# Optimization experiments

Hardware: AMD Instinct MI355X
Metric: run time of the kernel (lower is better)

The kernel has to match this reference:

```python
import jax, jax.numpy as jnp
import numpy as np

B, IN, H = 4096, 2048, 2048


def setup_inputs() -> dict:
    key = jax.random.key(0)
    ks = jax.random.split(key, 20)
    s_in = 1.0 / np.sqrt(IN)
    s_h = 1.0 / np.sqrt(H)
    inp = {
        "x": jax.random.normal(ks[0], (B, IN), jnp.float32),
        "h": jax.random.normal(ks[1], (B, H), jnp.float32),
        "c": jax.random.normal(ks[2], (B, H), jnp.float32),
    }
    names_in = [("Wii", "bii"), ("Wif", "bif"), ("Wig", "big"), ("Wio", "bio")]
    names_h = [("Whi", "bhi"), ("Whf", "bhf"), ("Whg", "bhg"), ("Who", "bho")]
    k = 3
    for wn, bn in names_in:
        inp[wn] = jax.random.normal(ks[k], (H, IN), jnp.float32) * s_in
        inp[bn] = jax.random.normal(ks[k + 1], (H,), jnp.float32) * s_in
        k += 2
    for wn, bn in names_h:
        inp[wn] = jax.random.normal(ks[k], (H, H), jnp.float32) * s_h
        inp[bn] = jax.random.normal(ks[k + 1], (H,), jnp.float32) * s_h
        k += 2
    return inp


def reference(x, h, c, Wii, bii, Whi, bhi, Wif, bif, Whf, bhf,
              Wig, big, Whg, bhg, Wio, bio, Who, bho):
    # Fuse the 4 input-projections and 4 hidden-projections into two GEMMs
    # (same math as 8 separate nn.Linear calls).
    Wx = jnp.concatenate([Wii, Wif, Wig, Wio], axis=0)   # [4H, IN]
    Wh = jnp.concatenate([Whi, Whf, Whg, Who], axis=0)   # [4H, H]
    bx = jnp.concatenate([bii, bif, big, bio])            # [4H]
    bh = jnp.concatenate([bhi, bhf, bhg, bho])            # [4H]
    gates = x @ Wx.T + h @ Wh.T + bx + bh                 # [B, 4H]
    ii, ff, gg, oo = jnp.split(gates, 4, axis=-1)
    i = jax.nn.sigmoid(ii)
    f = jax.nn.sigmoid(ff)
    g = jnp.tanh(gg)
    o = jax.nn.sigmoid(oo)
    c_new = f * c + i * g
    h_new = o * jnp.tanh(c_new)
    return jnp.stack([h_new, c_new])  # [2, B, H]
```

## Files before the change

### kernel.cpp

```cpp
#include <hip/hip_runtime.h>
#include <stdint.h>

typedef __attribute__((ext_vector_type(4))) float f32x4;
typedef __attribute__((ext_vector_type(8))) short bf16x8;

#define MFMA_BF16 __builtin_amdgcn_mfma_f32_16x16x32_bf16

__device__ __forceinline__ unsigned short f2bf(float f) {
  union { float f; uint32_t u; } a; a.f = f;
  uint32_t u = a.u;
  uint32_t r = (u + 0x7FFFu + ((u >> 16) & 1u)) >> 16;
  return (unsigned short)r;
}

__global__ void pack_a_kernel(const float4* __restrict__ x, const float4* __restrict__ hh,
                              ushort4* __restrict__ A) {
  const int total = 4096 * 1024;
  for (int q = blockIdx.x * blockDim.x + threadIdx.x; q < total; q += gridDim.x * blockDim.x) {
    int row = q >> 10, cq = q & 1023;
    float4 v = (cq < 512) ? x[row * 512 + cq] : hh[row * 512 + (cq - 512)];
    ushort4 o; o.x = f2bf(v.x); o.y = f2bf(v.y); o.z = f2bf(v.z); o.w = f2bf(v.w);
    A[q] = o;
  }
}

__global__ void pack_w_kernel(const float* __restrict__ Wii, const float* __restrict__ Wif,
                              const float* __restrict__ Wig, const float* __restrict__ Wio,
                              const float* __restrict__ Whi, const float* __restrict__ Whf,
                              const float* __restrict__ Whg, const float* __restrict__ Who,
                              ushort4* __restrict__ Wp) {
  const int total = 8192 * 1024;
  for (int q = blockIdx.x * blockDim.x + threadIdx.x; q < total; q += gridDim.x * blockDim.x) {
    int p = q >> 10, kq = q & 1023;
    int r = p & 255;
    int g = ((r >> 7) << 1) | ((r >> 4) & 1);
    int H = ((p >> 8) << 6) | (((r >> 5) & 3) << 4) | (r & 15);
    const float* src;
    if (kq < 512) src = (g == 0) ? Wii : (g == 1) ? Wif : (g == 2) ? Wig : Wio;
    else          src = (g == 0) ? Whi : (g == 1) ? Whf : (g == 2) ? Whg : Who;
    const float4 v = *(const float4*)&src[(size_t)H * 2048 + ((kq & 511) << 2)];
    ushort4 o; o.x = f2bf(v.x); o.y = f2bf(v.y); o.z = f2bf(v.z); o.w = f2bf(v.w);
    Wp[q] = o;
  }
}

#define STG(srcbase, jj, koff, dstE)                                                        \
  __builtin_amdgcn_global_load_lds(                                                        \
      (const __attribute__((address_space(1))) void*)((srcbase) + (size_t)(jj)*262144 + (koff)), \
      (__attribute__((address_space(3))) void*)(&smem[(dstE) + (jj)*4096]), 16, 0, 0)

__global__ __launch_bounds__(512, 2)
void lstm_gemm_kernel(const ushort* __restrict__ A, const ushort* __restrict__ Wp,
                      const float* __restrict__ c,
                      const float* __restrict__ bii, const float* __restrict__ bif_,
                      const float* __restrict__ big_, const float* __restrict__ bio_,
                      const float* __restrict__ bhi, const float* __restrict__ bhf,
                      const float* __restrict__ bhg, const float* __restrict__ bho,
                      float* __restrict__ out) {
  __shared__ ushort smem[65536];
  const int tid = threadIdx.x;
  const int lane = tid & 63, w = tid >> 6;
  const int wm = w >> 2, wn = w & 3;

  const int bid = blockIdx.x;
  const int xcd = bid & 7, q = bid >> 3;
  const int bn = (xcd << 2) | (q >> 4);
  const int bm = q & 15;

  const int laneRow = lane & 15, lane16 = lane >> 4;
  const int lr7 = laneRow & 7;
  const int colE0 = (lane16 ^ lr7) << 3;
  const int colE1 = ((4 + lane16) ^ lr7) << 3;

  const int srow = w * 8 + (lane >> 3);
  const int chunkOff = ((lane & 7) ^ (lane >> 3)) << 3;
  const ushort* aSrc = A + (size_t)(bm * 256 + srow) * 4096 + chunkOff;
  const ushort* bSrc = Wp + (size_t)(bn * 256 + srow) * 4096 + chunkOff;
  const int aDstW = w * 512;
  const int bDstW = 16384 + w * 512;

  const int aBase = (wm * 64 + laneRow) * 64;
  const int bBase = 16384 + (wn * 32 + laneRow) * 64;

  f32x4 acc[8][4];
#pragma unroll
  for (int i = 0; i < 8; i++)
#pragma unroll
    for (int j = 0; j < 4; j++) acc[i][j] = (f32x4){0.f, 0.f, 0.f, 0.f};

  STG(aSrc, 0, 0, aDstW); STG(aSrc, 1, 0, aDstW);
  STG(aSrc, 2, 0, aDstW); STG(aSrc, 3, 0, aDstW);
  STG(bSrc, 0, 0, bDstW); STG(bSrc, 1, 0, bDstW);
  STG(bSrc, 2, 0, bDstW); STG(bSrc, 3, 0, bDstW);
  asm volatile("s_waitcnt vmcnt(0)" ::: "memory");
  __builtin_amdgcn_s_barrier();
  __builtin_amdgcn_sched_barrier(0);

#pragma unroll 1
  for (int T = 0; T < 64; ++T) {
    const int bufE = (T & 1) << 15;
    const int obufE = bufE ^ 32768;
    const int kS = (T + 1) << 6;

    if (T < 63) {
      STG(aSrc, 0, kS, obufE + aDstW); STG(aSrc, 1, kS, obufE + aDstW);
      STG(aSrc, 2, kS, obufE + aDstW); STG(aSrc, 3, kS, obufE + aDstW);
      STG(bSrc, 0, kS, obufE + bDstW); STG(bSrc, 1, kS, obufE + bDstW);
      STG(bSrc, 2, kS, obufE + bDstW); STG(bSrc, 3, kS, obufE + bDstW);
    }

    bf16x8 af[4][2], b01[2][2], b23[2][2];
#pragma unroll
    for (int m = 0; m < 4; ++m) {
      af[m][0] = *(const bf16x8*)&smem[bufE + aBase + m * 1024 + colE0];
      af[m][1] = *(const bf16x8*)&smem[bufE + aBase + m * 1024 + colE1];
    }
#pragma unroll
    for (int n = 0; n < 2; ++n) {
      b01[n][0] = *(const bf16x8*)&smem[bufE + bBase + n * 1024 + colE0];
      b01[n][1] = *(const bf16x8*)&smem[bufE + bBase + n * 1024 + colE1];
    }
    __builtin_amdgcn_s_setprio(1);
#pragma unroll
    for (int m = 0; m < 4; ++m)
#pragma unroll
      for (int n = 0; n < 2; ++n) {
        acc[m][n] = MFMA_BF16(af[m][0], b01[n][0], acc[m][n], 0, 0, 0);
        acc[m][n] = MFMA_BF16(af[m][1], b01[n][1], acc[m][n], 0, 0, 0);
      }
    __builtin_amdgcn_s_setprio(0);

#pragma unroll
    for (int n = 0; n < 2; ++n) {
      b23[n][0] = *(const bf16x8*)&smem[bufE + bBase + 8192 + n * 1024 + colE0];
      b23[n][1] = *(const bf16x8*)&smem[bufE + bBase + 8192 + n * 1024 + colE1];
    }
    __builtin_amdgcn_s_setprio(1);
#pragma unroll
    for (int m = 0; m < 4; ++m)
#pragma unroll
      for (int n = 0; n < 2; ++n) {
        acc[m][2 + n] = MFMA_BF16(af[m][0], b23[n][0], acc[m][2 + n], 0, 0, 0);
        acc[m][2 + n] = MFMA_BF16(af[m][1], b23[n][1], acc[m][2 + n], 0, 0, 0);
      }
    __builtin_amdgcn_s_setprio(0);

#pragma unroll
    for (int m = 0; m < 4; ++m) {
      af[m][0] = *(const bf16x8*)&smem[bufE + aBase + 8192 + m * 1024 + colE0];
      af[m][1] = *(const bf16x8*)&smem[bufE + aBase + 8192 + m * 1024 + colE1];
    }
    __builtin_amdgcn_s_setprio(1);
#pragma unroll
    for (int m = 0; m < 4; ++m)
#pragma unroll
      for (int n = 0; n < 2; ++n) {
        acc[4 + m][n] = MFMA_BF16(af[m][0], b01[n][0], acc[4 + m][n], 0, 0, 0);
        acc[4 + m][n] = MFMA_BF16(af[m][1], b01[n][1], acc[4 + m][n], 0, 0, 0);
      }
    __builtin_amdgcn_s_setprio(0);

    __builtin_amdgcn_s_setprio(1);
#pragma unroll
    for (int m = 0; m < 4; ++m)
#pragma unroll
      for (int n = 0; n < 2; ++n) {
        acc[4 + m][2 + n] = MFMA_BF16(af[m][0], b23[n][0], acc[4 + m][2 + n], 0, 0, 0);
        acc[4 + m][2 + n] = MFMA_BF16(af[m][1], b23[n][1], acc[4 + m][2 + n], 0, 0, 0);
      }
    __builtin_amdgcn_s_setprio(0);

    asm volatile("s_waitcnt vmcnt(0)" ::: "memory");
    __builtin_amdgcn_s_barrier();
    __builtin_amdgcn_sched_barrier(0);
  }

  const int hcol = bn * 64 + wn * 16 + laneRow;
  const float bI = bii[hcol] + bhi[hcol];
  const float bF = bif_[hcol] + bhf[hcol];
  const float bG = big_[hcol] + bhg[hcol];
  const float bO = bio_[hcol] + bho[hcol];
#pragma unroll
  for (int mi = 0; mi < 8; ++mi) {
    const int rowBase = bm * 256 + (mi >> 2) * 128 + wm * 64 + (mi & 3) * 16 + lane16 * 4;
#pragma unroll
    for (int rr = 0; rr < 4; ++rr) {
      const int row = rowBase + rr;
      const float ii = acc[mi][0][rr] + bI;
      const float ff = acc[mi][1][rr] + bF;
      const float gg = acc[mi][2][rr] + bG;
      const float oo = acc[mi][3][rr] + bO;
      const float iv = 1.f / (1.f + __expf(-ii));
      const float fv = 1.f / (1.f + __expf(-ff));
      const float gv = tanhf(gg);
      const float ov = 1.f / (1.f + __expf(-oo));
      const float cv = c[(size_t)row * 2048 + hcol];
      const float cn = fv * cv + iv * gv;
      const float hn = ov * tanhf(cn);
      out[(size_t)row * 2048 + hcol] = hn;
      out[(size_t)8388608 + (size_t)row * 2048 + hcol] = cn;
    }
  }
}

extern "C" void kernel_launch(void* const* d_in, const int* in_sizes, int n_in,
                              void* d_out, int out_size, void* d_ws, size_t ws_size,
                              hipStream_t stream) {
  const float* x = (const float*)d_in[0];
  const float* h = (const float*)d_in[1];
  const float* c = (const float*)d_in[2];
  const float* Wii = (const float*)d_in[3];  const float* bii = (const float*)d_in[4];
  const float* Wif = (const float*)d_in[5];  const float* bif_ = (const float*)d_in[6];
  const float* Wig = (const float*)d_in[7];  const float* big_ = (const float*)d_in[8];
  const float* Wio = (const float*)d_in[9];  const float* bio_ = (const float*)d_in[10];
  const float* Whi = (const float*)d_in[11]; const float* bhi = (const float*)d_in[12];
  const float* Whf = (const float*)d_in[13]; const float* bhf = (const float*)d_in[14];
  const float* Whg = (const float*)d_in[15]; const float* bhg = (const float*)d_in[16];
  const float* Who = (const float*)d_in[17]; const float* bho = (const float*)d_in[18];

  ushort* Abf = (ushort*)d_ws;
  ushort* Wpk = Abf + (size_t)4096 * 4096;
  float* out = (float*)d_out;

  pack_a_kernel<<<2048, 256, 0, stream>>>((const float4*)x, (const float4*)h, (ushort4*)Abf);
  pack_w_kernel<<<2048, 256, 0, stream>>>(Wii, Wif, Wig, Wio, Whi, Whf, Whg, Who, (ushort4*)Wpk);
  lstm_gemm_kernel<<<512, 512, 0, stream>>>(Abf, Wpk, c,
                                            bii, bif_, big_, bio_, bhi, bhf, bhg, bho, out);
}
```

Measured before the change: 315.7 us.

## Switch GEMM main loop to 4-slot ring with K=32 steps and 3-deep prefetch

Replaces the double-buffered K=64 staging with a four-slot LDS ring of K=32 tiles. Loads are issued three stages ahead and only partially drained with vmcnt(8), so global-to-LDS traffic overlaps compute over a deeper window. The LDS layout and swizzle are reworked for the new 32-wide rows, and each step runs 32 MFMAs instead of 64. This doubles the number of barriers and iterations, and correctness depends on the new swizzle and the tail waitcnt logic.

Result: slower. 332.0 us (+5.2%).

```diff
diff --git a/kernel.cpp b/kernel.cpp
--- a/kernel.cpp
+++ b/kernel.cpp
@@ -44,10 +44,20 @@
   }
 }
 
-#define STG(srcbase, jj, koff, dstE)                                                        \
-  __builtin_amdgcn_global_load_lds(                                                        \
-      (const __attribute__((address_space(1))) void*)((srcbase) + (size_t)(jj)*262144 + (koff)), \
-      (__attribute__((address_space(3))) void*)(&smem[(dstE) + (jj)*4096]), 16, 0, 0)
+#define GLD(srcp, dstE)                                                         \
+  __builtin_amdgcn_global_load_lds(                                             \
+      (const __attribute__((address_space(1))) void*)(srcp),                    \
+      (__attribute__((address_space(3))) void*)(&smem[dstE]), 16, 0, 0)
+
+#define STAGE(t_)                                                               \
+  {                                                                             \
+    const int rr_ = ((t_) & 3) << 14;                                           \
+    const size_t kO_ = (size_t)(t_) * 32;                                       \
+    GLD(aS + kO_, rr_ + dA);                                                    \
+    GLD(aS + 524288 + kO_, rr_ + dA + 4096);                                    \
+    GLD(bS + kO_, rr_ + dB);                                                    \
+    GLD(bS + 524288 + kO_, rr_ + dB + 4096);                                    \
+  }
 
 __global__ __launch_bounds__(512, 2)
 void lstm_gemm_kernel(const ushort* __restrict__ A, const ushort* __restrict__ Wp,
@@ -63,24 +73,22 @@
   const int wm = w >> 2, wn = w & 3;
 
   const int bid = blockIdx.x;
-  const int xcd = bid & 7, q = bid >> 3;
-  const int bn = (xcd << 2) | (q >> 4);
-  const int bm = q & 15;
+  const int xcd = bid & 7, qq = bid >> 3;
+  const int bn = (xcd << 2) | (qq >> 4);
+  const int bm = qq & 15;
 
   const int laneRow = lane & 15, lane16 = lane >> 4;
-  const int lr7 = laneRow & 7;
-  const int colE0 = (lane16 ^ lr7) << 3;
-  const int colE1 = ((4 + lane16) ^ lr7) << 3;
+  const int chunkSwz = lane16 ^ ((laneRow >> 1) & 3);
+  const int rdCommon = (laneRow >> 1) * 64 + (laneRow & 1) * 32 + chunkSwz * 8;
+  const int aRB = wm * 2048 + rdCommon;
+  const int bRB = 8192 + wn * 1024 + rdCommon;
 
-  const int srow = w * 8 + (lane >> 3);
-  const int chunkOff = ((lane & 7) ^ (lane >> 3)) << 3;
-  const ushort* aSrc = A + (size_t)(bm * 256 + srow) * 4096 + chunkOff;
-  const ushort* bSrc = Wp + (size_t)(bn * 256 + srow) * 4096 + chunkOff;
-  const int aDstW = w * 512;
-  const int bDstW = 16384 + w * 512;
-
-  const int aBase = (wm * 64 + laneRow) * 64;
-  const int bBase = 16384 + (wn * 32 + laneRow) * 64;
+  const int lrow = 2 * (lane >> 3) + ((lane >> 2) & 1);
+  const int schunk = (lane & 3) ^ ((lane >> 3) & 3);
+  const ushort* aS = A + (size_t)(bm * 256 + 16 * w + lrow) * 4096 + schunk * 8;
+  const ushort* bS = Wp + (size_t)(bn * 256 + 16 * w + lrow) * 4096 + schunk * 8;
+  const int dA = w * 512;
+  const int dB = 8192 + w * 512;
 
   f32x4 acc[8][4];
 #pragma unroll
@@ -88,91 +96,48 @@
 #pragma unroll
     for (int j = 0; j < 4; j++) acc[i][j] = (f32x4){0.f, 0.f, 0.f, 0.f};
 
-  STG(aSrc, 0, 0, aDstW); STG(aSrc, 1, 0, aDstW);
-  STG(aSrc, 2, 0, aDstW); STG(aSrc, 3, 0, aDstW);
-  STG(bSrc, 0, 0, bDstW); STG(bSrc, 1, 0, bDstW);
-  STG(bSrc, 2, 0, bDstW); STG(bSrc, 3, 0, bDstW);
-  asm volatile("s_waitcnt vmcnt(0)" ::: "memory");
+  STAGE(0); STAGE(1); STAGE(2);
+  asm volatile("s_waitcnt vmcnt(8)" ::: "memory");
   __builtin_amdgcn_s_barrier();
   __builtin_amdgcn_sched_barrier(0);
 
 #pragma unroll 1
-  for (int T = 0; T < 64; ++T) {
-    const int bufE = (T & 1) << 15;
-    const int obufE = bufE ^ 32768;
-    const int kS = (T + 1) << 6;
+  for (int T = 0; T < 128; ++T) {
+    const int ring = (T & 3) << 14;
+    if (T < 125) STAGE(T + 3);
 
-    if (T < 63) {
-      STG(aSrc, 0, kS, obufE + aDstW); STG(aSrc, 1, kS, obufE + aDstW);
-      STG(aSrc, 2, kS, obufE + aDstW); STG(aSrc, 3, kS, obufE + aDstW);
-      STG(bSrc, 0, kS, obufE + bDstW); STG(bSrc, 1, kS, obufE + bDstW);
-      STG(bSrc, 2, kS, obufE + bDstW); STG(bSrc, 3, kS, obufE + bDstW);
-    }
-
-    bf16x8 af[4][2], b01[2][2], b23[2][2];
+    bf16x8 bf[4], af0[4], af1[4];
 #pragma unroll
-    for (int m = 0; m < 4; ++m) {
-      af[m][0] = *(const bf16x8*)&smem[bufE + aBase + m * 1024 + colE0];
-      af[m][1] = *(const bf16x8*)&smem[bufE + aBase + m * 1024 + colE1];
-    }
+    for (int ni = 0; ni < 4; ++ni)
+      bf[ni] = *(const bf16x8*)&smem[ring + bRB + (ni >> 1) * 4096 + (ni & 1) * 512];
 #pragma unroll
-    for (int n = 0; n < 2; ++n) {
-      b01[n][0] = *(const bf16x8*)&smem[bufE + bBase + n * 1024 + colE0];
-      b01[n][1] = *(const bf16x8*)&smem[bufE + bBase + n * 1024 + colE1];
-    }
+    for (int m = 0; m < 4; ++m)
+      af0[m] = *(const bf16x8*)&smem[ring + aRB + m * 512];
     __builtin_amdgcn_s_setprio(1);
 #pragma unroll
     for (int m = 0; m < 4; ++m)
 #pragma unroll
-      for (int n = 0; n < 2; ++n) {
-        acc[m][n] = MFMA_BF16(af[m][0], b01[n][0], acc[m][n], 0, 0, 0);
-        acc[m][n] = MFMA_BF16(af[m][1], b01[n][1], acc[m][n], 0, 0, 0);
-      }
+      for (int ni = 0; ni < 4; ++ni)
+        acc[m][ni] = MFMA_BF16(af0[m], bf[ni], acc[m][ni], 0, 0, 0);
     __builtin_amdgcn_s_setprio(0);
-
 #pragma unroll
-    for (int n = 0; n < 2; ++n) {
-      b23[n][0] = *(const bf16x8*)&smem[bufE + bBase + 8192 + n * 1024 + colE0];
-      b23[n][1] = *(const bf16x8*)&smem[bufE + bBase + 8192 + n * 1024 + colE1];
-    }
+    for (int m = 0; m < 4; ++m)
+      af1[m] = *(const bf16x8*)&smem[ring + aRB + 4096 + m * 512];
     __builtin_amdgcn_s_setprio(1);
 #pragma unroll
     for (int m = 0; m < 4; ++m)
 #pragma unroll
-      for (int n = 0; n < 2; ++n) {
-        acc[m][2 + n] = MFMA_BF16(af[m][0], b23[n][0], acc[m][2 + n], 0, 0, 0);
-        acc[m][2 + n] = MFMA_BF16(af[m][1], b23[n][1], acc[m][2 + n], 0, 0, 0);
-      }
+      for (int ni = 0; ni < 4; ++ni)
+        acc[4 + m][ni] = MFMA_BF16(af1[m], bf[ni], acc[4 + m][ni], 0, 0, 0);
     __builtin_amdgcn_s_setprio(0);
 
-#pragma unroll
-    for (int m = 0; m < 4; ++m) {
-      af[m][0] = *(const bf16x8*)&smem[bufE + aBase + 8192 + m * 1024 + colE0];
-      af[m][1] = *(const bf16x8*)&smem[bufE + aBase + 8192 + m * 1024 + colE1];
+    if (T < 125)       asm volatile("s_waitcnt vmcnt(8)" ::: "memory");
+    else if (T == 125) asm volatile("s_waitcnt vmcnt(4)" ::: "memory");
+    else if (T == 126) asm volatile("s_waitcnt vmcnt(0)" ::: "memory");
+    if (T < 127) {
+      __builtin_amdgcn_s_barrier();
+      __builtin_amdgcn_sched_barrier(0);
     }
-    __builtin_amdgcn_s_setprio(1);
-#pragma unroll
-    for (int m = 0; m < 4; ++m)
-#pragma unroll
-      for (int n = 0; n < 2; ++n) {
-        acc[4 + m][n] = MFMA_BF16(af[m][0], b01[n][0], acc[4 + m][n], 0, 0, 0);
-        acc[4 + m][n] = MFMA_BF16(af[m][1], b01[n][1], acc[4 + m][n], 0, 0, 0);
-      }
-    __builtin_amdgcn_s_setprio(0);
-
-    __builtin_amdgcn_s_setprio(1);
-#pragma unroll
-    for (int m = 0; m < 4; ++m)
-#pragma unroll
-      for (int n = 0; n < 2; ++n) {
-        acc[4 + m][2 + n] = MFMA_BF16(af[m][0], b23[n][0], acc[4 + m][2 + n], 0, 0, 0);
-        acc[4 + m][2 + n] = MFMA_BF16(af[m][1], b23[n][1], acc[4 + m][2 + n], 0, 0, 0);
-      }
-    __builtin_amdgcn_s_setprio(0);
-
-    asm volatile("s_waitcnt vmcnt(0)" ::: "memory");
-    __builtin_amdgcn_s_barrier();
-    __builtin_amdgcn_sched_barrier(0);
   }
 
   const int hcol = bn * 64 + wn * 16 + laneRow;
```
